# Kernel optimization log

Measured on AMD Instinct MI355X. Metric: run time of the kernel, lower is better.

## Reference

```python
import jax, jax.numpy as jnp
import numpy as np

N_IN = 25000     # source points
N_OUT = 25000    # query points
K = 32           # neighbors per query point
D_COORD = 3
D_FEAT = 64
D_HID = 128
D_OUT = 64


def setup_inputs() -> dict:
    key = jax.random.key(0)
    ks = jax.random.split(key, 8)
    y = jax.random.normal(ks[0], (N_IN, D_COORD), dtype=jnp.float32)
    x = jax.random.normal(ks[1], (N_OUT, D_COORD), dtype=jnp.float32)
    f_y = jax.random.normal(ks[2], (N_IN, D_FEAT), dtype=jnp.float32)
    d_in = 2 * D_COORD + D_FEAT  # 70
    W1 = jax.random.normal(ks[3], (d_in, D_HID), dtype=jnp.float32) / np.sqrt(d_in)
    b1 = jnp.zeros((D_HID,), dtype=jnp.float32)
    W2 = jax.random.normal(ks[4], (D_HID, D_OUT), dtype=jnp.float32) / np.sqrt(D_HID)
    b2 = jnp.zeros((D_OUT,), dtype=jnp.float32)
    a = jax.random.normal(ks[5], (D_HID,), dtype=jnp.float32) / np.sqrt(D_HID)
    neighbors_index = jax.random.randint(ks[6], (N_OUT * K,), 0, N_IN, dtype=jnp.int64)
    return {"y": y, "x": x, "f_y": f_y, "W1": W1, "b1": b1,
            "W2": W2, "b2": b2, "a": a, "neighbors_index": neighbors_index}


def reference(y, x, f_y, W1, b1, W2, b2, a, neighbors_index):
    E = neighbors_index.shape[0]           # N_OUT * K edges
    n_out = E // K
    # --- irregular gather of neighbor coords + features ---
    y_g = y[neighbors_index]               # [E, 3]
    f_g = f_y[neighbors_index]             # [E, 64]
    x_rep = jnp.repeat(x, K, axis=0)       # [E, 3]
    edge_in = jnp.concatenate([y_g, x_rep, f_g], axis=-1)  # [E, 70]
    # --- per-edge channel MLP ---
    h = jax.nn.gelu(edge_in @ W1 + b1)     # [E, 128]
    m = h @ W2 + b2                        # [E, 64]
    # --- attention weights, softmax within each neighborhood of K ---
    scores = (h @ a).reshape(n_out, K)     # [n_out, K]
    alpha = jax.nn.softmax(scores, axis=-1)
    # --- weighted scatter-reduce (regular K-block form) ---
    out = jnp.einsum('nk,nkd->nd', alpha, m.reshape(n_out, K, D_OUT))
    return out                             # [n_out, 64]
```

## Files before the change

kernel.cpp:

```cpp
#include <hip/hip_runtime.h>

typedef __attribute__((ext_vector_type(8))) short bf16x8;
typedef __attribute__((ext_vector_type(4))) float f32x4;

#define KNBR 32
#define WAVES 8

union Frag { int4 i; bf16x8 b; };

__device__ __forceinline__ unsigned short f2bf(float f) {
    unsigned u = __float_as_uint(f);
    u += 0x7FFFu + ((u >> 16) & 1u);
    return (unsigned short)(u >> 16);
}

__device__ __forceinline__ unsigned cvt_pk_bf16(float lo, float hi) {
    unsigned r;
    asm("v_cvt_pk_bf16_f32 %0, %1, %2" : "=v"(r) : "v"(lo), "v"(hi));
    return r;
}

__device__ __forceinline__ float fast_gelu(float v) {
    const float c1 = 0.044715f;
    const float K2 = -2.3022081951f;
    float p = v * fmaf(c1, v * v, 1.0f);
    float e, r;
    asm("v_exp_f32 %0, %1" : "=v"(e) : "v"(K2 * p));
    float d = 1.0f + e;
    asm("v_rcp_f32 %0, %1" : "=v"(r) : "v"(d));
    return v * r;
}

__global__ __launch_bounds__(256) void pack_weights_kernel(
    const float* __restrict__ W1, const float* __restrict__ W2,
    int4* __restrict__ W1p, int4* __restrict__ W2p)
{
    const int idx = blockIdx.x * 256 + threadIdx.x;
    unsigned short vals[8];
    if (idx < 1536) {
        const int r = idx >> 6, lane = idx & 63;
        const int mt = r / 3, s = r - mt * 3;
        const int row = mt * 16 + (lane & 15), g = lane >> 4;
        #pragma unroll
        for (int e = 0; e < 8; ++e) {
            const int k = s * 32 + g * 8 + e;
            float f;
            if      (k < 64) f = W1[(k + 6) * 128 + row];
            else if (k < 70) f = W1[(k - 64) * 128 + row];
            else             f = 0.0f;
            vals[e] = f2bf(f);
        }
        int4 v;
        v.x = vals[0] | (vals[1] << 16); v.y = vals[2] | (vals[3] << 16);
        v.z = vals[4] | (vals[5] << 16); v.w = vals[6] | (vals[7] << 16);
        W1p[idx] = v;
    } else if (idx < 2560) {
        const int i2 = idx - 1536;
        const int r = i2 >> 6, lane = i2 & 63;
        const int s = r >> 2, nt = r & 3;
        const int col = nt * 16 + (lane & 15), g = lane >> 4;
        #pragma unroll
        for (int e = 0; e < 8; ++e) {
            const int k = s * 32 + g * 4 + (e & 3) + 16 * (e >> 2);
            vals[e] = f2bf(W2[k * 64 + col]);
        }
        int4 v;
        v.x = vals[0] | (vals[1] << 16); v.y = vals[2] | (vals[3] << 16);
        v.z = vals[4] | (vals[5] << 16); v.w = vals[6] | (vals[7] << 16);
        W2p[i2] = v;
    }
}

__global__ __launch_bounds__(512, 6) void it_mfma_kernel(
    const float* __restrict__ y,
    const float* __restrict__ xq,
    const float* __restrict__ f_y,
    const float* __restrict__ b1,
    const float* __restrict__ b2,
    const float* __restrict__ av,
    const int*   __restrict__ nbr,
    const int4*  __restrict__ Wall,
    float*       __restrict__ out,
    int n_out)
{
    __shared__ int4 sW[2560];

    const int tid = threadIdx.x;
    const int w   = tid >> 6;
    const int l   = tid & 63;
    const int l15 = l & 15;
    const int g   = l >> 4;

    #pragma unroll
    for (int t = 0; t < 5; ++t)
        sW[tid + t * 512] = Wall[tid + t * 512];
    __syncthreads();
    const int4* sW1 = sW;
    const int4* sW2 = sW + 1536;

    const f32x4 zero4 = {0.f, 0.f, 0.f, 0.f};

    const int q = blockIdx.x * WAVES + w;
    if (q >= n_out) return;

    const int ni0 = nbr[q * KNBR + l15];
    const int ni1 = nbr[q * KNBR + 16 + l15];

    Frag B1[2][3];
    {
        const float4* f0 = (const float4*)(f_y + (long)ni0 * 64 + g * 8);
        const float4* f1 = (const float4*)(f_y + (long)ni1 * 64 + g * 8);
        float4 a0 = f0[0], a1 = f0[1];
        float4 a2 = f0[8], a3 = f0[9];
        float4 c0 = f1[0], c1 = f1[1];
        float4 c2 = f1[8], c3 = f1[9];
        B1[0][0].i.x = cvt_pk_bf16(a0.x, a0.y);
        B1[0][0].i.y = cvt_pk_bf16(a0.z, a0.w);
        B1[0][0].i.z = cvt_pk_bf16(a1.x, a1.y);
        B1[0][0].i.w = cvt_pk_bf16(a1.z, a1.w);
        B1[0][1].i.x = cvt_pk_bf16(a2.x, a2.y);
        B1[0][1].i.y = cvt_pk_bf16(a2.z, a2.w);
        B1[0][1].i.z = cvt_pk_bf16(a3.x, a3.y);
        B1[0][1].i.w = cvt_pk_bf16(a3.z, a3.w);
        B1[1][0].i.x = cvt_pk_bf16(c0.x, c0.y);
        B1[1][0].i.y = cvt_pk_bf16(c0.z, c0.w);
        B1[1][0].i.z = cvt_pk_bf16(c1.x, c1.y);
        B1[1][0].i.w = cvt_pk_bf16(c1.z, c1.w);
        B1[1][1].i.x = cvt_pk_bf16(c2.x, c2.y);
        B1[1][1].i.y = cvt_pk_bf16(c2.z, c2.w);
        B1[1][1].i.z = cvt_pk_bf16(c3.x, c3.y);
        B1[1][1].i.w = cvt_pk_bf16(c3.z, c3.w);
    }
    B1[0][2].i = make_int4(0, 0, 0, 0);
    B1[1][2].i = make_int4(0, 0, 0, 0);
    if (g == 0) {
        float2 ya = *(const float2*)(y + ni0 * 3);
        float  yaz = y[ni0 * 3 + 2];
        float2 yb = *(const float2*)(y + ni1 * 3);
        float  ybz = y[ni1 * 3 + 2];
        float2 x01 = *(const float2*)(xq + q * 3);
        float  xz  = xq[q * 3 + 2];
        B1[0][2].i.x = cvt_pk_bf16(ya.x, ya.y);
        B1[0][2].i.y = cvt_pk_bf16(yaz,  x01.x);
        B1[0][2].i.z = cvt_pk_bf16(x01.y, xz);
        B1[1][2].i.x = cvt_pk_bf16(yb.x, yb.y);
        B1[1][2].i.y = cvt_pk_bf16(ybz,  x01.x);
        B1[1][2].i.z = cvt_pk_bf16(x01.y, xz);
    }

    Frag A2[2][4];
    float sc0 = 0.f, sc1 = 0.f;
    #pragma unroll
    for (int j = 0; j < 4; ++j) {
        f32x4 acc[2][2] = {{zero4, zero4}, {zero4, zero4}};
        #pragma unroll
        for (int s = 0; s < 3; ++s) {
            Frag wa0, wa1;
            wa0.i = sW1[((2 * j + 0) * 3 + s) * 64 + l];
            wa1.i = sW1[((2 * j + 1) * 3 + s) * 64 + l];
            acc[0][0] = __builtin_amdgcn_mfma_f32_16x16x32_bf16(wa0.b, B1[0][s].b, acc[0][0], 0, 0, 0);
            acc[0][1] = __builtin_amdgcn_mfma_f32_16x16x32_bf16(wa0.b, B1[1][s].b, acc[0][1], 0, 0, 0);
            acc[1][0] = __builtin_amdgcn_mfma_f32_16x16x32_bf16(wa1.b, B1[0][s].b, acc[1][0], 0, 0, 0);
            acc[1][1] = __builtin_amdgcn_mfma_f32_16x16x32_bf16(wa1.b, B1[1][s].b, acc[1][1], 0, 0, 0);
        }
        #pragma unroll
        for (int mp = 0; mp < 2; ++mp) {
            const int hbase = (2 * j + mp) * 16 + g * 4;
            float4 b14 = *(const float4*)(b1 + hbase);
            float4 a14 = *(const float4*)(av + hbase);
            float h0[4], h1[4];
            h0[0] = fast_gelu(acc[mp][0][0] + b14.x);
            h0[1] = fast_gelu(acc[mp][0][1] + b14.y);
            h0[2] = fast_gelu(acc[mp][0][2] + b14.z);
            h0[3] = fast_gelu(acc[mp][0][3] + b14.w);
            h1[0] = fast_gelu(acc[mp][1][0] + b14.x);
            h1[1] = fast_gelu(acc[mp][1][1] + b14.y);
            h1[2] = fast_gelu(acc[mp][1][2] + b14.z);
            h1[3] = fast_gelu(acc[mp][1][3] + b14.w);
            sc0 = fmaf(h0[0], a14.x, sc0); sc0 = fmaf(h0[1], a14.y, sc0);
            sc0 = fmaf(h0[2], a14.z, sc0); sc0 = fmaf(h0[3], a14.w, sc0);
            sc1 = fmaf(h1[0], a14.x, sc1); sc1 = fmaf(h1[1], a14.y, sc1);
            sc1 = fmaf(h1[2], a14.z, sc1); sc1 = fmaf(h1[3], a14.w, sc1);
            if (mp == 0) {
                A2[0][j].i.x = cvt_pk_bf16(h0[0], h0[1]);
                A2[0][j].i.y = cvt_pk_bf16(h0[2], h0[3]);
                A2[1][j].i.x = cvt_pk_bf16(h1[0], h1[1]);
                A2[1][j].i.y = cvt_pk_bf16(h1[2], h1[3]);
            } else {
                A2[0][j].i.z = cvt_pk_bf16(h0[0], h0[1]);
                A2[0][j].i.w = cvt_pk_bf16(h0[2], h0[3]);
                A2[1][j].i.z = cvt_pk_bf16(h1[0], h1[1]);
                A2[1][j].i.w = cvt_pk_bf16(h1[2], h1[3]);
            }
        }
    }

    sc0 += __shfl_xor(sc0, 16, 64); sc0 += __shfl_xor(sc0, 32, 64);
    sc1 += __shfl_xor(sc1, 16, 64); sc1 += __shfl_xor(sc1, 32, 64);
    float mx = fmaxf(sc0, sc1);
    mx = fmaxf(mx, __shfl_xor(mx, 1, 64));
    mx = fmaxf(mx, __shfl_xor(mx, 2, 64));
    mx = fmaxf(mx, __shfl_xor(mx, 4, 64));
    mx = fmaxf(mx, __shfl_xor(mx, 8, 64));
    float ex0 = __expf(sc0 - mx);
    float ex1 = __expf(sc1 - mx);
    float sm = ex0 + ex1;
    sm += __shfl_xor(sm, 1, 64);
    sm += __shfl_xor(sm, 2, 64);
    sm += __shfl_xor(sm, 4, 64);
    sm += __shfl_xor(sm, 8, 64);
    const float inv = __fdividef(1.0f, sm);
    const float al0 = ex0 * inv;
    const float al1 = ex1 * inv;

    f32x4 acc2[2][4] = {{zero4, zero4, zero4, zero4},
                        {zero4, zero4, zero4, zero4}};
    #pragma unroll
    for (int s2 = 0; s2 < 4; ++s2) {
        #pragma unroll
        for (int nto = 0; nto < 4; ++nto) {
            Frag wb;
            wb.i = sW2[(s2 * 4 + nto) * 64 + l];
            acc2[0][nto] = __builtin_amdgcn_mfma_f32_16x16x32_bf16(A2[0][s2].b, wb.b, acc2[0][nto], 0, 0, 0);
            acc2[1][nto] = __builtin_amdgcn_mfma_f32_16x16x32_bf16(A2[1][s2].b, wb.b, acc2[1][nto], 0, 0, 0);
        }
    }

    float ar0[4], ar1[4];
    #pragma unroll
    for (int r = 0; r < 4; ++r) {
        ar0[r] = __shfl(al0, g * 4 + r, 64);
        ar1[r] = __shfl(al1, g * 4 + r, 64);
    }
    #pragma unroll
    for (int nto = 0; nto < 4; ++nto) {
        float o = 0.f;
        #pragma unroll
        for (int r = 0; r < 4; ++r) {
            o = fmaf(ar0[r], acc2[0][nto][r], o);
            o = fmaf(ar1[r], acc2[1][nto][r], o);
        }
        o += __shfl_xor(o, 16, 64);
        o += __shfl_xor(o, 32, 64);
        if (l < 16)
            out[q * 64 + nto * 16 + l] = o + b2[nto * 16 + l];
    }
}

extern "C" void kernel_launch(void* const* d_in, const int* in_sizes, int n_in,
                              void* d_out, int out_size, void* d_ws, size_t ws_size,
                              hipStream_t stream) {
    const float* y   = (const float*)d_in[0];
    const float* xq  = (const float*)d_in[1];
    const float* f_y = (const float*)d_in[2];
    const float* W1  = (const float*)d_in[3];
    const float* b1  = (const float*)d_in[4];
    const float* W2  = (const float*)d_in[5];
    const float* b2  = (const float*)d_in[6];
    const float* av  = (const float*)d_in[7];
    const int*   nbr = (const int*)d_in[8];
    float* out = (float*)d_out;

    const int n_out = in_sizes[1] / 3;

    int4* W1p = (int4*)d_ws;
    int4* W2p = W1p + 1536;

    pack_weights_kernel<<<10, 256, 0, stream>>>(W1, W2, W1p, W2p);
    const int nblk = (n_out + WAVES - 1) / WAVES;
    it_mfma_kernel<<<nblk, 512, 0, stream>>>(y, xq, f_y, b1, b2, av, nbr,
                                             W1p, out, n_out);
}
```

Before: 76.16 us.

## Switch per-edge MLP to 32x32x16 MFMA tiles and fold bias into K padding

Rewrites both GEMM stages to use 32x32x16 bf16 MFMA, so one 32-wide tile covers all 32 neighbors of a query. The weights are repacked for this layout, b1 is folded into the padded K slot via a constant 1.0 input, and the attention vector is pre-permuted into shared memory. This removes the per-element bias adds and halves the softmax bookkeeping, and pairs FMAs into packed form. In exchange, accumulators are larger (f32x16), and occupancy hints drop from 6 to 4 blocks, so register pressure and occupancy could change.

Result: faster. 72.05 us (-5.4%).

```diff
diff --git a/kernel.cpp b/kernel.cpp
--- a/kernel.cpp
+++ b/kernel.cpp
@@ -1,7 +1,8 @@
 #include <hip/hip_runtime.h>
 
-typedef __attribute__((ext_vector_type(8))) short bf16x8;
-typedef __attribute__((ext_vector_type(4))) float f32x4;
+typedef __attribute__((ext_vector_type(8)))  short bf16x8;
+typedef __attribute__((ext_vector_type(16))) float f32x16;
+typedef __attribute__((ext_vector_type(2)))  float f32x2;
 
 #define KNBR 32
 #define WAVES 8
@@ -33,217 +34,212 @@
 
 __global__ __launch_bounds__(256) void pack_weights_kernel(
     const float* __restrict__ W1, const float* __restrict__ W2,
-    int4* __restrict__ W1p, int4* __restrict__ W2p)
+    const float* __restrict__ b1, const float* __restrict__ av,
+    int4* __restrict__ W1p, int4* __restrict__ W2p, float* __restrict__ avp)
 {
     const int idx = blockIdx.x * 256 + threadIdx.x;
     unsigned short vals[8];
-    if (idx < 1536) {
-        const int r = idx >> 6, lane = idx & 63;
-        const int mt = r / 3, s = r - mt * 3;
-        const int row = mt * 16 + (lane & 15), g = lane >> 4;
+    if (idx < 1280) {
+        const int a = idx >> 6, l = idx & 63;
+        const int Mt = a / 5, ks = a - Mt * 5;
+        const int row = Mt * 32 + (l & 31), hi = l >> 5;
         #pragma unroll
         for (int e = 0; e < 8; ++e) {
-            const int k = s * 32 + g * 8 + e;
+            const int slot = ks * 16 + hi * 8 + e;
             float f;
-            if      (k < 64) f = W1[(k + 6) * 128 + row];
-            else if (k < 70) f = W1[(k - 64) * 128 + row];
-            else             f = 0.0f;
+            if      (slot < 64)  f = W1[(slot + 6) * 128 + row];
+            else if (slot < 70)  f = W1[(slot - 64) * 128 + row];
+            else if (slot == 70) f = b1[row];
+            else                 f = 0.0f;
             vals[e] = f2bf(f);
         }
         int4 v;
         v.x = vals[0] | (vals[1] << 16); v.y = vals[2] | (vals[3] << 16);
         v.z = vals[4] | (vals[5] << 16); v.w = vals[6] | (vals[7] << 16);
         W1p[idx] = v;
-    } else if (idx < 2560) {
-        const int i2 = idx - 1536;
-        const int r = i2 >> 6, lane = i2 & 63;
-        const int s = r >> 2, nt = r & 3;
-        const int col = nt * 16 + (lane & 15), g = lane >> 4;
+    } else if (idx < 2304) {
+        const int i2 = idx - 1280;
+        const int rgn = i2 >> 6, l = i2 & 63;
+        const int Nt = rgn >> 3, ks2 = rgn & 7;
+        const int col = Nt * 32 + (l & 31), hi = l >> 5;
         #pragma unroll
         for (int e = 0; e < 8; ++e) {
-            const int k = s * 32 + g * 4 + (e & 3) + 16 * (e >> 2);
-            vals[e] = f2bf(W2[k * 64 + col]);
+            const int Mt = ks2 >> 1;
+            const int t  = 2 * (ks2 & 1) + (e >> 2);
+            const int c  = e & 3;
+            const int hid = Mt * 32 + 4 * (2 * t + hi) + c;
+            vals[e] = f2bf(W2[hid * 64 + col]);
         }
         int4 v;
         v.x = vals[0] | (vals[1] << 16); v.y = vals[2] | (vals[3] << 16);
         v.z = vals[4] | (vals[5] << 16); v.w = vals[6] | (vals[7] << 16);
         W2p[i2] = v;
-    }
-}
-
-__global__ __launch_bounds__(512, 6) void it_mfma_kernel(
+    } else if (idx < 2432) {
+        const int r_ = idx - 2304;
+        const int Mt = r_ >> 5, hi = (r_ >> 4) & 1, r = r_ & 15;
+        avp[r_] = av[Mt * 32 + 8 * (r >> 2) + 4 * hi + (r & 3)];
+    }
+}
+
+__global__ __launch_bounds__(512, 4) void it_mfma_kernel(
     const float* __restrict__ y,
     const float* __restrict__ xq,
     const float* __restrict__ f_y,
-    const float* __restrict__ b1,
     const float* __restrict__ b2,
-    const float* __restrict__ av,
     const int*   __restrict__ nbr,
     const int4*  __restrict__ Wall,
     float*       __restrict__ out,
     int n_out)
 {
-    __shared__ int4 sW[2560];
+    __shared__ int4  sW[2304];
+    __shared__ float sAv[128];
 
     const int tid = threadIdx.x;
     const int w   = tid >> 6;
     const int l   = tid & 63;
-    const int l15 = l & 15;
-    const int g   = l >> 4;
-
-    #pragma unroll
-    for (int t = 0; t < 5; ++t)
-        sW[tid + t * 512] = Wall[tid + t * 512];
+    const int el  = l & 31;
+    const int hi  = l >> 5;
+
+    const int q = blockIdx.x * WAVES + w;
+    const bool active = (q < n_out);
+    const int qc = active ? q : 0;
+
+    const int ni = active ? nbr[qc * KNBR + el] : 0;
+
+    #pragma unroll
+    for (int t = 0; t < 5; ++t) {
+        const int idx = tid + t * 512;
+        if (idx < 2304) sW[idx] = Wall[idx];
+    }
+    if (tid < 128) sAv[tid] = ((const float*)(Wall + 2304))[tid];
     __syncthreads();
     const int4* sW1 = sW;
-    const int4* sW2 = sW + 1536;
-
-    const f32x4 zero4 = {0.f, 0.f, 0.f, 0.f};
-
-    const int q = blockIdx.x * WAVES + w;
-    if (q >= n_out) return;
-
-    const int ni0 = nbr[q * KNBR + l15];
-    const int ni1 = nbr[q * KNBR + 16 + l15];
-
-    Frag B1[2][3];
-    {
-        const float4* f0 = (const float4*)(f_y + (long)ni0 * 64 + g * 8);
-        const float4* f1 = (const float4*)(f_y + (long)ni1 * 64 + g * 8);
-        float4 a0 = f0[0], a1 = f0[1];
-        float4 a2 = f0[8], a3 = f0[9];
-        float4 c0 = f1[0], c1 = f1[1];
-        float4 c2 = f1[8], c3 = f1[9];
-        B1[0][0].i.x = cvt_pk_bf16(a0.x, a0.y);
-        B1[0][0].i.y = cvt_pk_bf16(a0.z, a0.w);
-        B1[0][0].i.z = cvt_pk_bf16(a1.x, a1.y);
-        B1[0][0].i.w = cvt_pk_bf16(a1.z, a1.w);
-        B1[0][1].i.x = cvt_pk_bf16(a2.x, a2.y);
-        B1[0][1].i.y = cvt_pk_bf16(a2.z, a2.w);
-        B1[0][1].i.z = cvt_pk_bf16(a3.x, a3.y);
-        B1[0][1].i.w = cvt_pk_bf16(a3.z, a3.w);
-        B1[1][0].i.x = cvt_pk_bf16(c0.x, c0.y);
-        B1[1][0].i.y = cvt_pk_bf16(c0.z, c0.w);
-        B1[1][0].i.z = cvt_pk_bf16(c1.x, c1.y);
-        B1[1][0].i.w = cvt_pk_bf16(c1.z, c1.w);
-        B1[1][1].i.x = cvt_pk_bf16(c2.x, c2.y);
-        B1[1][1].i.y = cvt_pk_bf16(c2.z, c2.w);
-        B1[1][1].i.z = cvt_pk_bf16(c3.x, c3.y);
-        B1[1][1].i.w = cvt_pk_bf16(c3.z, c3.w);
-    }
-    B1[0][2].i = make_int4(0, 0, 0, 0);
-    B1[1][2].i = make_int4(0, 0, 0, 0);
-    if (g == 0) {
-        float2 ya = *(const float2*)(y + ni0 * 3);
-        float  yaz = y[ni0 * 3 + 2];
-        float2 yb = *(const float2*)(y + ni1 * 3);
-        float  ybz = y[ni1 * 3 + 2];
-        float2 x01 = *(const float2*)(xq + q * 3);
-        float  xz  = xq[q * 3 + 2];
-        B1[0][2].i.x = cvt_pk_bf16(ya.x, ya.y);
-        B1[0][2].i.y = cvt_pk_bf16(yaz,  x01.x);
-        B1[0][2].i.z = cvt_pk_bf16(x01.y, xz);
-        B1[1][2].i.x = cvt_pk_bf16(yb.x, yb.y);
-        B1[1][2].i.y = cvt_pk_bf16(ybz,  x01.x);
-        B1[1][2].i.z = cvt_pk_bf16(x01.y, xz);
-    }
-
-    Frag A2[2][4];
-    float sc0 = 0.f, sc1 = 0.f;
-    #pragma unroll
-    for (int j = 0; j < 4; ++j) {
-        f32x4 acc[2][2] = {{zero4, zero4}, {zero4, zero4}};
-        #pragma unroll
-        for (int s = 0; s < 3; ++s) {
+    const int4* sW2 = sW + 1280;
+
+    if (!active) return;
+
+    const float4* fb = (const float4*)(f_y + (long)ni * 64);
+    float4 u0 = fb[ 0 + 2 * hi], u1 = fb[ 1 + 2 * hi];
+    float4 u2 = fb[ 4 + 2 * hi], u3 = fb[ 5 + 2 * hi];
+    float4 u4 = fb[ 8 + 2 * hi], u5 = fb[ 9 + 2 * hi];
+    float4 u6 = fb[12 + 2 * hi], u7 = fb[13 + 2 * hi];
+
+    Frag B1[5];
+    B1[0].i.x = cvt_pk_bf16(u0.x, u0.y); B1[0].i.y = cvt_pk_bf16(u0.z, u0.w);
+    B1[0].i.z = cvt_pk_bf16(u1.x, u1.y); B1[0].i.w = cvt_pk_bf16(u1.z, u1.w);
+    B1[1].i.x = cvt_pk_bf16(u2.x, u2.y); B1[1].i.y = cvt_pk_bf16(u2.z, u2.w);
+    B1[1].i.z = cvt_pk_bf16(u3.x, u3.y); B1[1].i.w = cvt_pk_bf16(u3.z, u3.w);
+    B1[2].i.x = cvt_pk_bf16(u4.x, u4.y); B1[2].i.y = cvt_pk_bf16(u4.z, u4.w);
+    B1[2].i.z = cvt_pk_bf16(u5.x, u5.y); B1[2].i.w = cvt_pk_bf16(u5.z, u5.w);
+    B1[3].i.x = cvt_pk_bf16(u6.x, u6.y); B1[3].i.y = cvt_pk_bf16(u6.z, u6.w);
+    B1[3].i.z = cvt_pk_bf16(u7.x, u7.y); B1[3].i.w = cvt_pk_bf16(u7.z, u7.w);
+    B1[4].i = make_int4(0, 0, 0, 0);
+    if (hi == 0) {
+        float2 y01 = *(const float2*)(y + ni * 3);
+        float  yz  = y[ni * 3 + 2];
+        float2 x01 = *(const float2*)(xq + qc * 3);
+        float  xz  = xq[qc * 3 + 2];
+        B1[4].i.x = cvt_pk_bf16(y01.x, y01.y);
+        B1[4].i.y = cvt_pk_bf16(yz,    x01.x);
+        B1[4].i.z = cvt_pk_bf16(x01.y, xz);
+        B1[4].i.w = cvt_pk_bf16(1.0f,  0.0f);
+    }
+
+    const f32x16 z16 = {0.f,0.f,0.f,0.f,0.f,0.f,0.f,0.f,
+                        0.f,0.f,0.f,0.f,0.f,0.f,0.f,0.f};
+
+    Frag A2[8];
+    f32x2 scv = {0.f, 0.f};
+    #pragma unroll
+    for (int p = 0; p < 2; ++p) {
+        f32x16 aA = z16, aB = z16;
+        #pragma unroll
+        for (int ks = 0; ks < 5; ++ks) {
             Frag wa0, wa1;
-            wa0.i = sW1[((2 * j + 0) * 3 + s) * 64 + l];
-            wa1.i = sW1[((2 * j + 1) * 3 + s) * 64 + l];
-            acc[0][0] = __builtin_amdgcn_mfma_f32_16x16x32_bf16(wa0.b, B1[0][s].b, acc[0][0], 0, 0, 0);
-            acc[0][1] = __builtin_amdgcn_mfma_f32_16x16x32_bf16(wa0.b, B1[1][s].b, acc[0][1], 0, 0, 0);
-            acc[1][0] = __builtin_amdgcn_mfma_f32_16x16x32_bf16(wa1.b, B1[0][s].b, acc[1][0], 0, 0, 0);
-            acc[1][1] = __builtin_amdgcn_mfma_f32_16x16x32_bf16(wa1.b, B1[1][s].b, acc[1][1], 0, 0, 0);
-        }
-        #pragma unroll
-        for (int mp = 0; mp < 2; ++mp) {
-            const int hbase = (2 * j + mp) * 16 + g * 4;
-            float4 b14 = *(const float4*)(b1 + hbase);
-            float4 a14 = *(const float4*)(av + hbase);
-            float h0[4], h1[4];
-            h0[0] = fast_gelu(acc[mp][0][0] + b14.x);
-            h0[1] = fast_gelu(acc[mp][0][1] + b14.y);
-            h0[2] = fast_gelu(acc[mp][0][2] + b14.z);
-            h0[3] = fast_gelu(acc[mp][0][3] + b14.w);
-            h1[0] = fast_gelu(acc[mp][1][0] + b14.x);
-            h1[1] = fast_gelu(acc[mp][1][1] + b14.y);
-            h1[2] = fast_gelu(acc[mp][1][2] + b14.z);
-            h1[3] = fast_gelu(acc[mp][1][3] + b14.w);
-            sc0 = fmaf(h0[0], a14.x, sc0); sc0 = fmaf(h0[1], a14.y, sc0);
-            sc0 = fmaf(h0[2], a14.z, sc0); sc0 = fmaf(h0[3], a14.w, sc0);
-            sc1 = fmaf(h1[0], a14.x, sc1); sc1 = fmaf(h1[1], a14.y, sc1);
-            sc1 = fmaf(h1[2], a14.z, sc1); sc1 = fmaf(h1[3], a14.w, sc1);
-            if (mp == 0) {
-                A2[0][j].i.x = cvt_pk_bf16(h0[0], h0[1]);
-                A2[0][j].i.y = cvt_pk_bf16(h0[2], h0[3]);
-                A2[1][j].i.x = cvt_pk_bf16(h1[0], h1[1]);
-                A2[1][j].i.y = cvt_pk_bf16(h1[2], h1[3]);
-            } else {
-                A2[0][j].i.z = cvt_pk_bf16(h0[0], h0[1]);
-                A2[0][j].i.w = cvt_pk_bf16(h0[2], h0[3]);
-                A2[1][j].i.z = cvt_pk_bf16(h1[0], h1[1]);
-                A2[1][j].i.w = cvt_pk_bf16(h1[2], h1[3]);
+            wa0.i = sW1[((2 * p + 0) * 5 + ks) * 64 + l];
+            wa1.i = sW1[((2 * p + 1) * 5 + ks) * 64 + l];
+            aA = __builtin_amdgcn_mfma_f32_32x32x16_bf16(wa0.b, B1[ks].b, aA, 0, 0, 0);
+            aB = __builtin_amdgcn_mfma_f32_32x32x16_bf16(wa1.b, B1[ks].b, aB, 0, 0, 0);
+        }
+        #pragma unroll
+        for (int m = 0; m < 2; ++m) {
+            const f32x16 ac = m ? aB : aA;
+            const int Mt = 2 * p + m;
+            const float* avb = sAv + Mt * 32 + hi * 16;
+            float4 av0 = *(const float4*)(avb + 0);
+            float4 av1 = *(const float4*)(avb + 4);
+            float4 av2 = *(const float4*)(avb + 8);
+            float4 av3 = *(const float4*)(avb + 12);
+            float avr[16] = {av0.x, av0.y, av0.z, av0.w,
+                             av1.x, av1.y, av1.z, av1.w,
+                             av2.x, av2.y, av2.z, av2.w,
+                             av3.x, av3.y, av3.z, av3.w};
+            float h[16];
+            #pragma unroll
+            for (int r = 0; r < 16; ++r) h[r] = fast_gelu(ac[r]);
+            #pragma unroll
+            for (int i = 0; i < 8; ++i) {
+                f32x2 hv = {h[2 * i], h[2 * i + 1]};
+                f32x2 avv = {avr[2 * i], avr[2 * i + 1]};
+                scv = __builtin_elementwise_fma(hv, avv, scv);
             }
-        }
-    }
-
-    sc0 += __shfl_xor(sc0, 16, 64); sc0 += __shfl_xor(sc0, 32, 64);
-    sc1 += __shfl_xor(sc1, 16, 64); sc1 += __shfl_xor(sc1, 32, 64);
-    float mx = fmaxf(sc0, sc1);
+            A2[2 * Mt + 0].i.x = cvt_pk_bf16(h[0],  h[1]);
+            A2[2 * Mt + 0].i.y = cvt_pk_bf16(h[2],  h[3]);
+            A2[2 * Mt + 0].i.z = cvt_pk_bf16(h[4],  h[5]);
+            A2[2 * Mt + 0].i.w = cvt_pk_bf16(h[6],  h[7]);
+            A2[2 * Mt + 1].i.x = cvt_pk_bf16(h[8],  h[9]);
+            A2[2 * Mt + 1].i.y = cvt_pk_bf16(h[10], h[11]);
+            A2[2 * Mt + 1].i.z = cvt_pk_bf16(h[12], h[13]);
+            A2[2 * Mt + 1].i.w = cvt_pk_bf16(h[14], h[15]);
+        }
+    }
+
+    float sc = scv.x + scv.y;
+    sc += __shfl_xor(sc, 32, 64);
+    float mx = sc;
     mx = fmaxf(mx, __shfl_xor(mx, 1, 64));
     mx = fmaxf(mx, __shfl_xor(mx, 2, 64));
     mx = fmaxf(mx, __shfl_xor(mx, 4, 64));
     mx = fmaxf(mx, __shfl_xor(mx, 8, 64));
-    float ex0 = __expf(sc0 - mx);
-    float ex1 = __expf(sc1 - mx);
-    float sm = ex0 + ex1;
+    mx = fmaxf(mx, __shfl_xor(mx, 16, 64));
+    float ex = __expf(sc - mx);
+    float sm = ex;
     sm += __shfl_xor(sm, 1, 64);
     sm += __shfl_xor(sm, 2, 64);
     sm += __shfl_xor(sm, 4, 64);
     sm += __shfl_xor(sm, 8, 64);
-    const float inv = __fdividef(1.0f, sm);
-    const float al0 = ex0 * inv;
-    const float al1 = ex1 * inv;
-
-    f32x4 acc2[2][4] = {{zero4, zero4, zero4, zero4},
-                        {zero4, zero4, zero4, zero4}};
-    #pragma unroll
-    for (int s2 = 0; s2 < 4; ++s2) {
-        #pragma unroll
-        for (int nto = 0; nto < 4; ++nto) {
-            Frag wb;
-            wb.i = sW2[(s2 * 4 + nto) * 64 + l];
-            acc2[0][nto] = __builtin_amdgcn_mfma_f32_16x16x32_bf16(A2[0][s2].b, wb.b, acc2[0][nto], 0, 0, 0);
-            acc2[1][nto] = __builtin_amdgcn_mfma_f32_16x16x32_bf16(A2[1][s2].b, wb.b, acc2[1][nto], 0, 0, 0);
-        }
-    }
-
-    float ar0[4], ar1[4];
-    #pragma unroll
-    for (int r = 0; r < 4; ++r) {
-        ar0[r] = __shfl(al0, g * 4 + r, 64);
-        ar1[r] = __shfl(al1, g * 4 + r, 64);
-    }
-    #pragma unroll
-    for (int nto = 0; nto < 4; ++nto) {
-        float o = 0.f;
-        #pragma unroll
-        for (int r = 0; r < 4; ++r) {
-            o = fmaf(ar0[r], acc2[0][nto][r], o);
-            o = fmaf(ar1[r], acc2[1][nto][r], o);
-        }
-        o += __shfl_xor(o, 16, 64);
+    sm += __shfl_xor(sm, 16, 64);
+    const float alpha = __fdividef(ex, sm);
+
+    f32x16 o0 = z16, o1 = z16;
+    #pragma unroll
+    for (int ks2 = 0; ks2 < 8; ++ks2) {
+        Frag w0, w1;
+        w0.i = sW2[(0 * 8 + ks2) * 64 + l];
+        w1.i = sW2[(1 * 8 + ks2) * 64 + l];
+        o0 = __builtin_amdgcn_mfma_f32_32x32x16_bf16(A2[ks2].b, w0.b, o0, 0, 0, 0);
+        o1 = __builtin_amdgcn_mfma_f32_32x32x16_bf16(A2[ks2].b, w1.b, o1, 0, 0, 0);
+    }
+
+    float ar[16];
+    #pragma unroll
+    for (int r = 0; r < 16; ++r)
+        ar[r] = __shfl(alpha, 8 * (r >> 2) + 4 * hi + (r & 3), 64);
+
+    #pragma unroll
+    for (int nt = 0; nt < 2; ++nt) {
+        const f32x16 oo = nt ? o1 : o0;
+        f32x2 acc = {0.f, 0.f};
+        #pragma unroll
+        for (int i = 0; i < 8; ++i) {
+            f32x2 ov = {oo[2 * i], oo[2 * i + 1]};
+            f32x2 av2 = {ar[2 * i], ar[2 * i + 1]};
+            acc = __builtin_elementwise_fma(ov, av2, acc);
+        }
+        float o = acc.x + acc.y;
         o += __shfl_xor(o, 32, 64);
-        if (l < 16)
-            out[q * 64 + nto * 16 + l] = o + b2[nto * 16 + l];
+        if (l < 32)
+            out[qc * 64 + nt * 32 + l] = o + b2[nt * 32 + l];
     }
 }
 
@@ -263,11 +259,12 @@
 
     const int n_out = in_sizes[1] / 3;
 
-    int4* W1p = (int4*)d_ws;
-    int4* W2p = W1p + 1536;
-
-    pack_weights_kernel<<<10, 256, 0, stream>>>(W1, W2, W1p, W2p);
+    int4*  W1p = (int4*)d_ws;
+    int4*  W2p = W1p + 1280;
+    float* avp = (float*)(W1p + 2304);
+
+    pack_weights_kernel<<<10, 256, 0, stream>>>(W1, W2, b1, av, W1p, W2p, avp);
     const int nblk = (n_out + WAVES - 1) / WAVES;
-    it_mfma_kernel<<<nblk, 512, 0, stream>>>(y, xq, f_y, b1, b2, av, nbr,
+    it_mfma_kernel<<<nblk, 512, 0, stream>>>(y, xq, f_y, b2, nbr,
                                              W1p, out, n_out);
 }
```
